# Kernel optimization log

Hardware: AMD Instinct MI355X
Metric: run time of the kernel (lower is better)

The kernel has to match this reference:

```python
import jax, jax.numpy as jnp
import numpy as np


def setup_inputs() -> dict:
    key = jax.random.key(0)
    b, c, h, w = 16, 64, 256, 256
    x = jax.random.normal(key, (b, c, h, w), dtype=jnp.float32)
    gamma = jnp.ones((1,), dtype=jnp.float32)
    return {"x": x, "gamma": gamma}


def reference(x, gamma):
    # Channel self-attention: scores are CxC, softmax over (max - score).
    b, c, h, w = x.shape
    q = x.reshape(b, c, h * w)                      # [b, c, N] (query==key==value)
    att = jnp.einsum('bcn,bdn->bcd', q, q)          # [b, c, c] = Q @ K^T
    # reversed softmax: rowwise max minus scores, then softmax over last dim
    rev = jnp.max(att, axis=-1, keepdims=True) - att
    att_sm = jax.nn.softmax(rev, axis=-1)           # [b, c, c]
    res = jnp.einsum('bcd,bdn->bcn', att_sm, q)     # [b, c, N]
    res = res.reshape(b, c, h, w)
    return gamma * res + x
```

## Files before the change

kernel.cpp:

```cpp
#include <hip/hip_runtime.h>
#include <math.h>


#define CH 64
#define NPIX 65536

__global__ __launch_bounds__(256, 2) void ca_gram_kernel(
    const float* __restrict__ x, float* __restrict__ partials) {
  __shared__ float lds[4][4096];
  const int b    = blockIdx.y;
  const int wave = threadIdx.x >> 6;
  const int lane = threadIdx.x & 63;
  const int tx   = lane & 7;
  const int ty   = (lane >> 3) & 7;
  const int nblk = lane & 15;
  const int r0   = lane >> 4;
  const int k    = blockIdx.x * 4 + wave;
  const float* qb = x + (size_t)b * CH * NPIX;
  float* tile = lds[wave];

  float acc[8][8];
#pragma unroll
  for (int m = 0; m < 8; ++m)
#pragma unroll
    for (int p = 0; p < 8; ++p) acc[m][p] = 0.f;

  float4 pre[16];
#pragma unroll
  for (int m = 0; m < 16; ++m) {
    const int c = r0 * 16 + m;
    pre[m] = *(const float4*)(qb + (size_t)c * NPIX + k * 512 + nblk * 4);
  }

  for (int t = 0; t < 8; ++t) {
#pragma unroll
    for (int m = 0; m < 16; ++m) {
      const int c = r0 * 16 + m;
      *(float4*)(tile + c * 64 + ((nblk ^ (m & 7)) << 2)) = pre[m];
    }
    if (t < 7) {
#pragma unroll
      for (int m = 0; m < 16; ++m) {
        const int c = r0 * 16 + m;
        pre[m] = *(const float4*)(qb + (size_t)c * NPIX + k * 512 + (t + 1) * 64 + nblk * 4);
      }
    }
    for (int g = 0; g < 16; ++g) {
      float4 a4[8], b4[8];
#pragma unroll
      for (int m = 0; m < 8; ++m) {
        a4[m] = *(const float4*)(tile + (tx + 8 * m) * 64 + ((g ^ tx) << 2));
        b4[m] = *(const float4*)(tile + (ty + 8 * m) * 64 + ((g ^ ty) << 2));
      }
#pragma unroll
      for (int m = 0; m < 8; ++m)
#pragma unroll
        for (int p = 0; p < 8; ++p)
          acc[m][p] = fmaf(a4[m].x, b4[p].x,
                      fmaf(a4[m].y, b4[p].y,
                      fmaf(a4[m].z, b4[p].z,
                      fmaf(a4[m].w, b4[p].w, acc[m][p]))));
    }
  }
#pragma unroll
  for (int m = 0; m < 8; ++m)
#pragma unroll
    for (int p = 0; p < 8; ++p)
      tile[(tx + 8 * m) * 64 + (ty + 8 * p)] = acc[m][p];
  __syncthreads();
  float* outp = partials + (size_t)(b * 32 + blockIdx.x) * 4096;
  for (int i = threadIdx.x; i < 4096; i += 256)
    outp[i] = lds[0][i] + lds[1][i] + lds[2][i] + lds[3][i];
}

__global__ void ca_softmax_kernel(const float* __restrict__ partials,
                                  const float* __restrict__ gamma,
                                  float* __restrict__ ApT) {
  const int b = blockIdx.y, c = blockIdx.x, d = threadIdx.x;
  const float* p = partials + (size_t)b * 32 * 4096 + c * 64 + d;
  float s = 0.f;
#pragma unroll
  for (int kk = 0; kk < 32; ++kk) s += p[(size_t)kk * 4096];
  float mn = s;
#pragma unroll
  for (int off = 32; off > 0; off >>= 1) mn = fminf(mn, __shfl_down(mn, off));
  mn = __shfl(mn, 0);
  const float w = expf(mn - s);
  float sum = w;
#pragma unroll
  for (int off = 32; off > 0; off >>= 1) sum += __shfl_down(sum, off);
  sum = __shfl(sum, 0);
  const float v = gamma[0] * (w / sum) + (c == d ? 1.f : 0.f);
  ApT[((size_t)b * 64 + d) * 64 + c] = v;
}

__global__ __launch_bounds__(256, 2) void ca_apply_kernel(
    const float* __restrict__ x, const float* __restrict__ ApT,
    float* __restrict__ out) {
  __shared__ float At[4096];
  const int b    = blockIdx.y;
  const int tid  = threadIdx.x;
  const int wave = tid >> 6;
  const int lane = tid & 63;
  const int c0   = wave * 16;

  const float* src = ApT + (size_t)b * 4096;
#pragma unroll
  for (int i = 0; i < 4; ++i)
    ((float4*)At)[tid + 256 * i] = ((const float4*)src)[tid + 256 * i];
  __syncthreads();

  const size_t pix = (size_t)blockIdx.x * 256 + lane * 4;
  const float* xb = x + (size_t)b * CH * NPIX + pix;
  float4 acc[16];
#pragma unroll
  for (int c = 0; c < 16; ++c) acc[c] = make_float4(0.f, 0.f, 0.f, 0.f);

  for (int d0 = 0; d0 < 64; d0 += 4) {
    float4 xv[4];
#pragma unroll
    for (int j = 0; j < 4; ++j)
      xv[j] = *(const float4*)(xb + (size_t)(d0 + j) * NPIX);
#pragma unroll
    for (int j = 0; j < 4; ++j) {
#pragma unroll
      for (int q = 0; q < 4; ++q) {
        const float4 a = *(const float4*)(At + (d0 + j) * 64 + c0 + q * 4);
        const float av[4] = {a.x, a.y, a.z, a.w};
#pragma unroll
        for (int e = 0; e < 4; ++e) {
          float4& A4 = acc[q * 4 + e];
          A4.x = fmaf(av[e], xv[j].x, A4.x);
          A4.y = fmaf(av[e], xv[j].y, A4.y);
          A4.z = fmaf(av[e], xv[j].z, A4.z);
          A4.w = fmaf(av[e], xv[j].w, A4.w);
        }
      }
    }
  }
  float* ob = out + (size_t)b * CH * NPIX + pix;
#pragma unroll
  for (int c = 0; c < 16; ++c)
    *(float4*)(ob + (size_t)(c0 + c) * NPIX) = acc[c];
}

extern "C" void kernel_launch(void* const* d_in, const int* in_sizes, int n_in,
                              void* d_out, int out_size, void* d_ws, size_t ws_size,
                              hipStream_t stream) {
  const float* x     = (const float*)d_in[0];
  const float* gamma = (const float*)d_in[1];
  float* out      = (float*)d_out;
  float* partials = (float*)d_ws;
  float* ApT      = partials + (size_t)512 * 4096;

  ca_gram_kernel<<<dim3(32, 16), 256, 0, stream>>>(x, partials);
  ca_softmax_kernel<<<dim3(64, 16), 64, 0, stream>>>(partials, gamma, ApT);
  ca_apply_kernel<<<dim3(256, 16), 256, 0, stream>>>(x, ApT, out);
}
```

Before: 634.1 us.

## Compute Gram matrix with split-bf16 MFMA instead of scalar FP32 FMAs

```diff
diff --git a/kernel.cpp b/kernel.cpp
--- a/kernel.cpp
+++ b/kernel.cpp
@@ -5,72 +5,100 @@
 #define CH 64
 #define NPIX 65536
 
+typedef __bf16 bf16x8 __attribute__((ext_vector_type(8)));
+typedef float f32x16 __attribute__((ext_vector_type(16)));
+
 __global__ __launch_bounds__(256, 2) void ca_gram_kernel(
     const float* __restrict__ x, float* __restrict__ partials) {
-  __shared__ float lds[4][4096];
+  __shared__ unsigned short Hp[2][64 * 128];
+  __shared__ unsigned short Lp[2][64 * 128];
   const int b    = blockIdx.y;
-  const int wave = threadIdx.x >> 6;
-  const int lane = threadIdx.x & 63;
-  const int tx   = lane & 7;
-  const int ty   = (lane >> 3) & 7;
-  const int nblk = lane & 15;
-  const int r0   = lane >> 4;
-  const int k    = blockIdx.x * 4 + wave;
+  const int tid  = threadIdx.x;
+  const int wave = tid >> 6;
+  const int lane = tid & 63;
+  const int r    = lane & 31;
+  const int half = lane >> 5;
+  const int ti   = wave >> 1, tj = wave & 1;
   const float* qb = x + (size_t)b * CH * NPIX;
-  float* tile = lds[wave];
+  const int px0 = blockIdx.x * 2048;
+  const int sc  = tid >> 5;
+  const int sp  = (tid & 31) * 4;
 
-  float acc[8][8];
+  f32x16 accHH, accHL;
 #pragma unroll
-  for (int m = 0; m < 8; ++m)
+  for (int q = 0; q < 16; ++q) { accHH[q] = 0.f; accHL[q] = 0.f; }
+
+  float4 pre[8];
 #pragma unroll
-    for (int p = 0; p < 8; ++p) acc[m][p] = 0.f;
+  for (int i2 = 0; i2 < 8; ++i2)
+    pre[i2] = *(const float4*)(qb + (size_t)(i2 * 8 + sc) * NPIX + px0 + sp);
 
-  float4 pre[16];
+  const int rowA = ti * 32 + r;
+  const int rowB = tj * 32 + r;
+
+  for (int t = 0; t < 16; ++t) {
+    unsigned short* hw = Hp[t & 1];
+    unsigned short* lw = Lp[t & 1];
 #pragma unroll
-  for (int m = 0; m < 16; ++m) {
-    const int c = r0 * 16 + m;
-    pre[m] = *(const float4*)(qb + (size_t)c * NPIX + k * 512 + nblk * 4);
+    for (int i2 = 0; i2 < 8; ++i2) {
+      const int c = i2 * 8 + sc;
+      const float vv[4] = {pre[i2].x, pre[i2].y, pre[i2].z, pre[i2].w};
+      unsigned int hb[4], lb[4];
+#pragma unroll
+      for (int e = 0; e < 4; ++e) {
+        const unsigned int u = __float_as_uint(vv[e]);
+        hb[e] = (u + 0x7FFFu + ((u >> 16) & 1u)) >> 16;
+        const float lf = vv[e] - __uint_as_float(hb[e] << 16);
+        const unsigned int ul = __float_as_uint(lf);
+        lb[e] = (ul + 0x7FFFu + ((ul >> 16) & 1u)) >> 16;
+      }
+      const int g   = sp >> 3;
+      const int off = c * 128 + (((g ^ (c & 15)) << 3) | (sp & 7));
+      *(uint2*)(hw + off) = make_uint2(hb[0] | (hb[1] << 16), hb[2] | (hb[3] << 16));
+      *(uint2*)(lw + off) = make_uint2(lb[0] | (lb[1] << 16), lb[2] | (lb[3] << 16));
+    }
+    __syncthreads();
+
+    if (t < 15) {
+#pragma unroll
+      for (int i2 = 0; i2 < 8; ++i2)
+        pre[i2] = *(const float4*)(qb + (size_t)(i2 * 8 + sc) * NPIX + px0 +
+                                   (t + 1) * 128 + sp);
+    }
+
+    const unsigned short* hr = Hp[t & 1];
+    const unsigned short* lr = Lp[t & 1];
+#pragma unroll
+    for (int ks = 0; ks < 8; ++ks) {
+      const int g = ks * 2 + half;
+      const bf16x8 aH = *(const bf16x8*)(hr + rowA * 128 + ((g ^ (rowA & 15)) << 3));
+      bf16x8 bH;
+      if (ti == tj) bH = aH;
+      else bH = *(const bf16x8*)(hr + rowB * 128 + ((g ^ (rowB & 15)) << 3));
+      const bf16x8 bL = *(const bf16x8*)(lr + rowB * 128 + ((g ^ (rowB & 15)) << 3));
+      accHH = __builtin_amdgcn_mfma_f32_32x32x16_bf16(aH, bH, accHH, 0, 0, 0);
+      accHL = __builtin_amdgcn_mfma_f32_32x32x16_bf16(aH, bL, accHL, 0, 0, 0);
+    }
   }
 
-  for (int t = 0; t < 8; ++t) {
+  float mine[16];
 #pragma unroll
-    for (int m = 0; m < 16; ++m) {
-      const int c = r0 * 16 + m;
-      *(float4*)(tile + c * 64 + ((nblk ^ (m & 7)) << 2)) = pre[m];
-    }
-    if (t < 7) {
+  for (int q = 0; q < 16; ++q) mine[q] = 0.5f * accHH[q] + accHL[q];
+  float* ep = (float*)&Hp[0][0];
 #pragma unroll
-      for (int m = 0; m < 16; ++m) {
-        const int c = r0 * 16 + m;
-        pre[m] = *(const float4*)(qb + (size_t)c * NPIX + k * 512 + (t + 1) * 64 + nblk * 4);
-      }
-    }
-    for (int g = 0; g < 16; ++g) {
-      float4 a4[8], b4[8];
+  for (int q = 0; q < 16; ++q) {
+    const int row = (q & 3) + 8 * (q >> 2) + 4 * half;
+    ep[wave * 1024 + row * 32 + (r ^ row)] = mine[q];
+  }
+  __syncthreads();
+  const int ptile = tj * 2 + ti;
+  float* outp = partials + (size_t)(b * 32 + blockIdx.x) * 4096;
 #pragma unroll
-      for (int m = 0; m < 8; ++m) {
-        a4[m] = *(const float4*)(tile + (tx + 8 * m) * 64 + ((g ^ tx) << 2));
-        b4[m] = *(const float4*)(tile + (ty + 8 * m) * 64 + ((g ^ ty) << 2));
-      }
-#pragma unroll
-      for (int m = 0; m < 8; ++m)
-#pragma unroll
-        for (int p = 0; p < 8; ++p)
-          acc[m][p] = fmaf(a4[m].x, b4[p].x,
-                      fmaf(a4[m].y, b4[p].y,
-                      fmaf(a4[m].z, b4[p].z,
-                      fmaf(a4[m].w, b4[p].w, acc[m][p]))));
-    }
+  for (int q = 0; q < 16; ++q) {
+    const int row = (q & 3) + 8 * (q >> 2) + 4 * half;
+    const float theirs = ep[ptile * 1024 + r * 32 + (row ^ r)];
+    outp[(32 * ti + row) * 64 + 32 * tj + r] = mine[q] + theirs;
   }
-#pragma unroll
-  for (int m = 0; m < 8; ++m)
-#pragma unroll
-    for (int p = 0; p < 8; ++p)
-      tile[(tx + 8 * m) * 64 + (ty + 8 * p)] = acc[m][p];
-  __syncthreads();
-  float* outp = partials + (size_t)(b * 32 + blockIdx.x) * 4096;
-  for (int i = threadIdx.x; i < 4096; i += 256)
-    outp[i] = lds[0][i] + lds[1][i] + lds[2][i] + lds[3][i];
 }
 
 __global__ void ca_softmax_kernel(const float* __restrict__ partials,
```

After: 565.6 us. 1.12x faster.

## Compute Gram matrix with bf16 split-precision MFMA instead of fp32 FMA

Applied to the files above, without the earlier changes.

```diff
diff --git a/kernel.cpp b/kernel.cpp
--- a/kernel.cpp
+++ b/kernel.cpp
@@ -4,73 +4,108 @@
 
 #define CH 64
 #define NPIX 65536
+#define PITCH 48
+
+typedef __bf16 bf16x8 __attribute__((ext_vector_type(8)));
+typedef float f32x4 __attribute__((ext_vector_type(4)));
 
 __global__ __launch_bounds__(256, 2) void ca_gram_kernel(
     const float* __restrict__ x, float* __restrict__ partials) {
-  __shared__ float lds[4][4096];
+  __shared__ __align__(16) unsigned char smem[65536];
   const int b    = blockIdx.y;
-  const int wave = threadIdx.x >> 6;
-  const int lane = threadIdx.x & 63;
-  const int tx   = lane & 7;
-  const int ty   = (lane >> 3) & 7;
-  const int nblk = lane & 15;
-  const int r0   = lane >> 4;
-  const int k    = blockIdx.x * 4 + wave;
+  const int tid  = threadIdx.x;
+  const int wave = tid >> 6;
+  const int lane = tid & 63;
+  const int cho    = lane >> 3;
+  const int px_off = (lane & 7) * 4;
+  const int gw     = px_off >> 3;
+  const int ha     = px_off & 4;
+  const int r16 = lane & 15;
+  const int g16 = lane >> 4;
+
+  unsigned short* Ht = (unsigned short*)smem + wave * (2 * 64 * PITCH);
+  unsigned short* Lt = Ht + 64 * PITCH;
+
   const float* qb = x + (size_t)b * CH * NPIX;
-  float* tile = lds[wave];
+  const size_t px_base = (size_t)blockIdx.x * 2048 + wave * 512;
 
-  float acc[8][8];
+  f32x4 acc[4][4];
+#pragma unroll
+  for (int i = 0; i < 4; ++i)
+#pragma unroll
+    for (int j = 0; j < 4; ++j) acc[i][j] = (f32x4)(0.f);
+
+  float4 pre[8];
 #pragma unroll
   for (int m = 0; m < 8; ++m)
+    pre[m] = *(const float4*)(qb + (size_t)(m * 8 + cho) * NPIX + px_base + px_off);
+
+  for (int s = 0; s < 16; ++s) {
 #pragma unroll
-    for (int p = 0; p < 8; ++p) acc[m][p] = 0.f;
-
-  float4 pre[16];
+    for (int m = 0; m < 8; ++m) {
+      const int ch = m * 8 + cho;
+      const float vv[4] = {pre[m].x, pre[m].y, pre[m].z, pre[m].w};
+      unsigned short hu[4], lu[4];
 #pragma unroll
-  for (int m = 0; m < 16; ++m) {
-    const int c = r0 * 16 + m;
-    pre[m] = *(const float4*)(qb + (size_t)c * NPIX + k * 512 + nblk * 4);
+      for (int e = 0; e < 4; ++e) {
+        const __bf16 hb = (__bf16)vv[e];
+        const float  hf = (float)hb;
+        const __bf16 lb = (__bf16)(2.f * (vv[e] - hf));
+        hu[e] = __builtin_bit_cast(unsigned short, hb);
+        lu[e] = __builtin_bit_cast(unsigned short, lb);
+      }
+      const int wa = ch * PITCH + (((gw ^ (ch & 3)) << 3) | ha);
+      *(uint2*)(Ht + wa) = make_uint2(hu[0] | (hu[1] << 16), hu[2] | (hu[3] << 16));
+      *(uint2*)(Lt + wa) = make_uint2(lu[0] | (lu[1] << 16), lu[2] | (lu[3] << 16));
+    }
+    if (s < 15) {
+#pragma unroll
+      for (int m = 0; m < 8; ++m)
+        pre[m] = *(const float4*)(qb + (size_t)(m * 8 + cho) * NPIX + px_base +
+                                  (s + 1) * 32 + px_off);
+    }
+    bf16x8 aH[4], aL[4];
+#pragma unroll
+    for (int i = 0; i < 4; ++i) {
+      const int ra = (i * 16 + r16) * PITCH + ((g16 ^ (r16 & 3)) << 3);
+      aH[i] = *(const bf16x8*)(Ht + ra);
+      aL[i] = *(const bf16x8*)(Lt + ra);
+    }
+#pragma unroll
+    for (int i = 0; i < 4; ++i)
+#pragma unroll
+      for (int j = 0; j < 4; ++j) {
+        acc[i][j] = __builtin_amdgcn_mfma_f32_16x16x32_bf16(aH[i], aH[j], acc[i][j], 0, 0, 0);
+        acc[i][j] = __builtin_amdgcn_mfma_f32_16x16x32_bf16(aH[i], aL[j], acc[i][j], 0, 0, 0);
+      }
   }
 
-  for (int t = 0; t < 8; ++t) {
+  __syncthreads();
+  float* ep = (float*)smem + wave * 4096;
 #pragma unroll
-    for (int m = 0; m < 16; ++m) {
-      const int c = r0 * 16 + m;
-      *(float4*)(tile + c * 64 + ((nblk ^ (m & 7)) << 2)) = pre[m];
-    }
-    if (t < 7) {
+  for (int i = 0; i < 4; ++i)
 #pragma unroll
-      for (int m = 0; m < 16; ++m) {
-        const int c = r0 * 16 + m;
-        pre[m] = *(const float4*)(qb + (size_t)c * NPIX + k * 512 + (t + 1) * 64 + nblk * 4);
+    for (int j = 0; j < 4; ++j)
+#pragma unroll
+      for (int q = 0; q < 4; ++q) {
+        const int R = i * 16 + g16 * 4 + q;
+        const int C = j * 16 + r16;
+        ep[R * 64 + (C & 48) + ((C ^ R) & 15)] = acc[i][j][q];
       }
-    }
-    for (int g = 0; g < 16; ++g) {
-      float4 a4[8], b4[8];
-#pragma unroll
-      for (int m = 0; m < 8; ++m) {
-        a4[m] = *(const float4*)(tile + (tx + 8 * m) * 64 + ((g ^ tx) << 2));
-        b4[m] = *(const float4*)(tile + (ty + 8 * m) * 64 + ((g ^ ty) << 2));
-      }
-#pragma unroll
-      for (int m = 0; m < 8; ++m)
-#pragma unroll
-        for (int p = 0; p < 8; ++p)
-          acc[m][p] = fmaf(a4[m].x, b4[p].x,
-                      fmaf(a4[m].y, b4[p].y,
-                      fmaf(a4[m].z, b4[p].z,
-                      fmaf(a4[m].w, b4[p].w, acc[m][p]))));
-    }
-  }
-#pragma unroll
-  for (int m = 0; m < 8; ++m)
-#pragma unroll
-    for (int p = 0; p < 8; ++p)
-      tile[(tx + 8 * m) * 64 + (ty + 8 * p)] = acc[m][p];
   __syncthreads();
   float* outp = partials + (size_t)(b * 32 + blockIdx.x) * 4096;
-  for (int i = threadIdx.x; i < 4096; i += 256)
-    outp[i] = lds[0][i] + lds[1][i] + lds[2][i] + lds[3][i];
+  for (int k = 0; k < 16; ++k) {
+    const int idx = k * 256 + tid;
+    const int r = idx >> 6, c = idx & 63;
+    float ssum = 0.f;
+#pragma unroll
+    for (int w = 0; w < 4; ++w) {
+      const float* epw = (float*)smem + w * 4096;
+      ssum += epw[r * 64 + (c & 48) + ((c ^ r) & 15)]
+            + epw[c * 64 + (r & 48) + ((r ^ c) & 15)];
+    }
+    outp[idx] = 0.5f * ssum;
+  }
 }
 
 __global__ void ca_softmax_kernel(const float* __restrict__ partials,
```

New measurement: 552.3 us. -12.9%, faster.
